# Kernel optimization log

Hardware: AMD Instinct MI355X
Metric: run time of the kernel (lower is better)

## Reference

```python
import jax, jax.numpy as jnp
import numpy as np

B, S, T = 2, 4096, 4096
SRC, DST, WIDTH = 512, 512, 128
BLK = 128  # JAKAL_ADDITIVE_ROUTE_BLOCK_SIZE default


def setup_inputs() -> dict:
    key = jax.random.key(0)
    ks = jax.random.split(key, 7)
    return {
        "source_val": jax.random.normal(ks[0], (B, S, SRC), jnp.float32),
        "target_val": jax.random.normal(ks[1], (B, T, DST), jnp.float32),
        "Ws": jax.random.normal(ks[2], (WIDTH, SRC), jnp.float32) * 0.02,  # source_proj weight
        "Wt": jax.random.normal(ks[3], (WIDTH, DST), jnp.float32) * 0.02,  # target_proj weight
        "ws_out": jax.random.normal(ks[4], (WIDTH,), jnp.float32) * 0.02,  # source_out weight
        "wt_out": jax.random.normal(ks[5], (WIDTH,), jnp.float32) * 0.02,  # target_out weight
        "w_int": jax.random.normal(ks[6], (WIDTH,), jnp.float32) * 0.02,   # interaction_weight
        "bias": jnp.zeros((), jnp.float32),
    }


def reference(source_val, target_val, Ws, Wt, ws_out, wt_out, w_int, bias):
    # Projections (Linear without bias): y = x @ W.T
    ps = jnp.einsum('bsd,wd->bsw', source_val, Ws)   # [B,S,WIDTH]
    pt = jnp.einsum('btd,wd->btw', target_val, Wt)   # [B,T,WIDTH]
    s_lin = jnp.einsum('bsw,w->bs', ps, ws_out)      # [B,S]
    t_lin = jnp.einsum('btw,w->bt', pt, wt_out)      # [B,T]

    nblk = S // BLK
    # Block the source axis, matching the torch block loop (avoids a [B,S,T,W] tensor).
    ps_blocks = ps.reshape(B, nblk, BLK, WIDTH).transpose(1, 0, 2, 3)   # [nblk,B,BLK,W]
    sl_blocks = s_lin.reshape(B, nblk, BLK).transpose(1, 0, 2)          # [nblk,B,BLK]

    def block_scores(_, xs):
        ps_blk, sl_blk = xs
        # SiLU of the elementwise bilinear interaction, then low-rank weighted reduce.
        inter = jax.nn.silu(ps_blk[:, :, None, :] * pt[:, None, :, :])  # [B,BLK,T,W]
        sc = jnp.einsum('bktw,w->bkt', inter, w_int)
        sc = sc + sl_blk[:, :, None] + t_lin[:, None, :] + bias
        return None, sc

    _, out = jax.lax.scan(block_scores, None, (ps_blocks, sl_blocks))   # [nblk,B,BLK,T]
    return out.transpose(1, 0, 2, 3).reshape(B, S, T)
```

## Files before the change

### kernel.cpp

```cpp
#include <hip/hip_runtime.h>
#include <cstdint>
#include <cstddef>

#define B_ 2
#define S_ 4096
#define T_ 4096
#define D_ 512
#define W_ 128

#define A0C (-0.0006958f)
#define A1C (0.2529946f)
#define A2C (-0.0226345f)
#define A3C (0.0022173f)
#define A4C (-0.00011668f)
#define ZCUT 2.5f
#define ROWCAP 65536

typedef __attribute__((ext_vector_type(8))) short bf16x8;
typedef __attribute__((ext_vector_type(4))) float f32x4;

__device__ __forceinline__ uint16_t f2bf(float f){
  uint32_t u = __float_as_uint(f);
  u += 0x7FFFu + ((u >> 16) & 1u);
  return (uint16_t)(u >> 16);
}
__device__ __forceinline__ float bf2f(uint16_t h){
  return __uint_as_float(((uint32_t)h) << 16);
}

__device__ __forceinline__ void gl_lds16(const void* g, void* l){
  __builtin_amdgcn_global_load_lds(
      (const __attribute__((address_space(1))) void*)g,
      (__attribute__((address_space(3))) void*)l, 16, 0, 0);
}

union F4 { float4 v; float f[4]; };

template<int INBF>
__global__ void prep_k(const void* __restrict__ Ws, const void* __restrict__ Wt,
                       const void* __restrict__ wso, const void* __restrict__ wto,
                       const void* __restrict__ wi, const void* __restrict__ bias,
                       float* __restrict__ WsT, float* __restrict__ WtT,
                       float* __restrict__ wsof, float* __restrict__ wtof,
                       float* __restrict__ wif, float* __restrict__ cbias,
                       float* __restrict__ maxT, int* __restrict__ rowCnt){
  auto cv = [](const void* p, int i)->float{
    if (INBF) return bf2f(((const uint16_t*)p)[i]);
    return ((const float*)p)[i];
  };
  const void* in = (blockIdx.x & 1) ? Wt : Ws;
  float* out = (blockIdx.x & 1) ? WtT : WsT;
  int base = (blockIdx.x >> 1) * 4096;
  for (int o = base + threadIdx.x; o < base + 4096; o += blockDim.x){
    int d = o >> 7, w = o & (W_ - 1);
    out[o] = cv(in, w * D_ + d);
  }
  if (blockIdx.x == 1){
    maxT[threadIdx.x] = 0.f;
  }
  if (blockIdx.x == 0){
    if (threadIdx.x < W_){
      wsof[threadIdx.x] = cv(wso, threadIdx.x);
      wtof[threadIdx.x] = cv(wto, threadIdx.x);
      wif[threadIdx.x]  = cv(wi,  threadIdx.x);
    }
    __syncthreads();
    if (threadIdx.x == 0){
      float s = 0.f;
      for (int k = 0; k < W_; ++k) s += wif[k];
      cbias[0] = cv(bias, 0) + A0C * s;
      rowCnt[0] = 0;
    }
  }
}

template<int INBF, int MODE>
__global__ __launch_bounds__(256) void proj_k(const void* __restrict__ xraw,
        const float* __restrict__ WT, const float* __restrict__ wout,
        const float* __restrict__ wint,
        float* __restrict__ pT, float* __restrict__ lin,
        uint16_t* __restrict__ feat, float* __restrict__ maxT){
  __shared__ float xl[64 * 18];
  __shared__ float wl[64 * 128];
  int tid = threadIdx.x;
  int tx = tid & 31, ty = tid >> 5;
  int rowBase = blockIdx.x * 16;
  float acc[2][4] = {};
  for (int c = 0; c < 8; ++c){
    int d0 = c * 64;
    const float4* wt4 = (const float4*)(WT + (size_t)d0 * W_);
    float4* wl4 = (float4*)wl;
    #pragma unroll
    for (int p = 0; p < 8; ++p){ int q = tid + 256 * p; wl4[q] = wt4[q]; }
    {
      int q = tid;
      int r = q >> 4, dq = q & 15;
      float v0, v1, v2, v3;
      if (INBF){
        const uint16_t* xp = (const uint16_t*)xraw + (size_t)(rowBase + r) * D_ + d0 + dq * 4;
        ushort4 u = *(const ushort4*)xp;
        v0 = bf2f(u.x); v1 = bf2f(u.y); v2 = bf2f(u.z); v3 = bf2f(u.w);
      } else {
        const float* xp = (const float*)xraw + (size_t)(rowBase + r) * D_ + d0 + dq * 4;
        float4 u = *(const float4*)xp;
        v0 = u.x; v1 = u.y; v2 = u.z; v3 = u.w;
      }
      xl[(dq*4+0)*18 + r] = v0;
      xl[(dq*4+1)*18 + r] = v1;
      xl[(dq*4+2)*18 + r] = v2;
      xl[(dq*4+3)*18 + r] = v3;
    }
    __syncthreads();
    #pragma unroll 4
    for (int d = 0; d < 64; ++d){
      float a0 = xl[d * 18 + ty * 2 + 0];
      float a1 = xl[d * 18 + ty * 2 + 1];
      F4 w;
      w.v = *(const float4*)(wl + d * 128 + tx * 4);
      #pragma unroll
      for (int j = 0; j < 4; ++j){
        acc[0][j] = fmaf(a0, w.f[j], acc[0][j]);
        acc[1][j] = fmaf(a1, w.f[j], acc[1][j]);
      }
    }
    __syncthreads();
  }
  float* tile = wl;
  #pragma unroll
  for (int i = 0; i < 2; ++i)
    #pragma unroll
    for (int j = 0; j < 4; ++j)
      tile[(tx*4 + j) * 17 + ty*2 + i] = acc[i][j];
  F4 wo; wo.v = *(const float4*)(wout + tx * 4);
  F4 wiv;
  if (MODE == 0) wiv.v = *(const float4*)(wint + tx * 4);
  #pragma unroll
  for (int i = 0; i < 2; ++i){
    int r = rowBase + ty * 2 + i;
    float s = acc[i][0]*wo.f[0] + acc[i][1]*wo.f[1] + acc[i][2]*wo.f[2] + acc[i][3]*wo.f[3];
    #pragma unroll
    for (int off = 16; off >= 1; off >>= 1) s += __shfl_xor(s, off, 32);
    if (tx == 0) lin[r] = s;
    ushort4 g[5];
    uint16_t* gp = (uint16_t*)g;
    #pragma unroll
    for (int j = 0; j < 4; ++j){
      float p = acc[i][j];
      float p2 = p*p, p4 = p2*p2, p6 = p4*p2, p8 = p4*p4;
      float e0, e1, e2, e3, e4;
      if (MODE == 0){
        float wq = wiv.f[j];
        e0 = 0.5f * wq * p; e1 = A1C * wq * p2; e2 = A2C * wq * p4;
        e3 = A3C * wq * p6; e4 = A4C * wq * p8;
      } else {
        e0 = p; e1 = p2; e2 = p4; e3 = p6; e4 = p8;
      }
      gp[0*4+j] = f2bf(e0); gp[1*4+j] = f2bf(e1); gp[2*4+j] = f2bf(e2);
      gp[3*4+j] = f2bf(e3); gp[4*4+j] = f2bf(e4);
    }
    uint16_t* o = feat + (size_t)r * 640 + tx * 4;
    *(ushort4*)(o)       = g[0];
    *(ushort4*)(o + 128) = g[1];
    *(ushort4*)(o + 256) = g[2];
    *(ushort4*)(o + 384) = g[3];
    *(ushort4*)(o + 512) = g[4];
  }
  __syncthreads();
  int b = rowBase >> 12;
  {
    int w = tid >> 1, h = tid & 1;
    int sb = rowBase & (S_ - 1);
    float* dst = pT + ((size_t)(b * W_ + w)) * S_ + sb + h * 8;
    const float* src = tile + w * 17 + h * 8;
    #pragma unroll
    for (int k = 0; k < 2; ++k){
      float4 o = make_float4(src[k*4+0], src[k*4+1], src[k*4+2], src[k*4+3]);
      *(float4*)(dst + k * 4) = o;
    }
  }
  if (MODE == 1 && tid < W_){
    int w = tid;
    float m = 0.f;
    #pragma unroll
    for (int r = 0; r < 16; ++r) m = fmaxf(m, fabsf(tile[w * 17 + r]));
    atomicMax((unsigned int*)&maxT[b * W_ + w], __float_as_uint(m));
  }
}

template<int OUTBF>
__global__ __launch_bounds__(512) void gemm_k(const uint16_t* __restrict__ fA,
      const uint16_t* __restrict__ fB, const float* __restrict__ slin,
      const float* __restrict__ tlin, const float* __restrict__ cbias,
      void* __restrict__ outv){
  __shared__ __align__(16) uint16_t As[2][256 * 32];
  __shared__ __align__(16) uint16_t Bs[2][256 * 32];
  int tid = threadIdx.x, lane = tid & 63, wv = tid >> 6;
  int quad = lane >> 4, lr = lane & 15;
  int wm = wv >> 2, wn = wv & 3;
  int sl = quad ^ ((lane >> 1) & 3);
  int rowT = blockIdx.y * 256, colT = blockIdx.x * 256;
  int bb = rowT >> 12;

  const uint16_t* aBase = fA + (size_t)rowT * 640;
  const uint16_t* bBase = fB + ((size_t)bb * T_ + colT) * 640;

  int srw = tid >> 2;
  int k0 = (((tid & 3) ^ ((tid >> 3) & 3))) * 8;

  f32x4 acc[8][4];
  #pragma unroll
  for (int i = 0; i < 8; ++i)
    #pragma unroll
    for (int j = 0; j < 4; ++j)
      acc[i][j] = (f32x4){0.f, 0.f, 0.f, 0.f};

  auto STAGE = [&](int tile){
    int sb = tile & 1;
    int kc = tile * 32;
    gl_lds16(aBase + (size_t)srw * 640 + kc + k0,         &As[sb][tid * 8]);
    gl_lds16(aBase + (size_t)(128 + srw) * 640 + kc + k0, &As[sb][4096 + tid * 8]);
    gl_lds16(bBase + (size_t)srw * 640 + kc + k0,         &Bs[sb][tid * 8]);
    gl_lds16(bBase + (size_t)(128 + srw) * 640 + kc + k0, &Bs[sb][4096 + tid * 8]);
  };

  STAGE(0);
  for (int tile = 0; tile < 20; ++tile){
    int buf = tile & 1;
    if (tile + 1 < 20){
      STAGE(tile + 1);
      asm volatile("s_waitcnt vmcnt(4)" ::: "memory");
    } else {
      asm volatile("s_waitcnt vmcnt(0)" ::: "memory");
    }
    __builtin_amdgcn_s_barrier();
    bf16x8 bq[4];
    #pragma unroll
    for (int nj = 0; nj < 4; ++nj)
      bq[nj] = *(const bf16x8*)&Bs[buf][(wn*64 + nj*16 + lr) * 32 + sl * 8];
    #pragma unroll
    for (int mi = 0; mi < 8; ++mi){
      bf16x8 aq = *(const bf16x8*)&As[buf][(wm*128 + mi*16 + lr) * 32 + sl * 8];
      #pragma unroll
      for (int nj = 0; nj < 4; ++nj)
        acc[mi][nj] = __builtin_amdgcn_mfma_f32_16x16x32_bf16(bq[nj], aq, acc[mi][nj], 0, 0, 0);
    }
    __builtin_amdgcn_s_barrier();
  }

  float cb = cbias[0];
  #pragma unroll
  for (int mi = 0; mi < 8; ++mi){
    int srow = rowT + wm * 128 + mi * 16 + lr;
    float sv = slin[srow] + cb;
    #pragma unroll
    for (int nj = 0; nj < 4; ++nj){
      int t0 = colT + wn * 64 + nj * 16 + quad * 4;
      F4 tl; tl.v = *(const float4*)(tlin + bb * T_ + t0);
      float o0 = acc[mi][nj][0] + sv + tl.f[0];
      float o1 = acc[mi][nj][1] + sv + tl.f[1];
      float o2 = acc[mi][nj][2] + sv + tl.f[2];
      float o3 = acc[mi][nj][3] + sv + tl.f[3];
      size_t oi = (size_t)srow * T_ + t0;
      if (OUTBF){
        ushort4 pk = make_ushort4(f2bf(o0), f2bf(o1), f2bf(o2), f2bf(o3));
        *(ushort4*)((uint16_t*)outv + oi) = pk;
      } else {
        *(float4*)((float*)outv + oi) = make_float4(o0, o1, o2, o3);
      }
    }
  }
}

__global__ void flagrows_k(const float* __restrict__ psT, const float* __restrict__ maxT,
                           uint32_t* __restrict__ rowList, int* __restrict__ rowCnt){
  int w = blockIdx.x, b = blockIdx.y;
  int tid = threadIdx.x;
  float mt = maxT[b * W_ + w];
  const float* psc = psT + (size_t)(b * W_ + w) * S_;
  for (int s = tid; s < S_; s += 256){
    float p = psc[s];
    if (fabsf(p) * mt > ZCUT){
      int k = atomicAdd(rowCnt, 1);
      if (k < ROWCAP)
        rowList[k] = ((uint32_t)b << 19) | ((uint32_t)w << 12) | (uint32_t)s;
    }
  }
}

template<int OUTBF>
__global__ __launch_bounds__(256) void fixscan_k(const float* __restrict__ psT,
        const float* __restrict__ ptT, const float* __restrict__ wint,
        const uint16_t* __restrict__ fA, const uint16_t* __restrict__ fB,
        const uint32_t* __restrict__ rowList, const int* __restrict__ rowCnt,
        void* __restrict__ outv){
  int n = *rowCnt; if (n > ROWCAP) n = ROWCAP;
  int tid = threadIdx.x;
  for (int job = blockIdx.x; job < n; job += gridDim.x){
    uint32_t pk = rowList[job];
    int b = (int)(pk >> 19), w = (int)((pk >> 12) & 127u), s = (int)(pk & 4095u);
    float wi = wint[w];
    float p = psT[(size_t)(b * W_ + w) * S_ + s];
    const float* ptc = ptT + (size_t)(b * W_ + w) * T_;
    const uint16_t* fa = fA + ((size_t)b * S_ + s) * 640 + w;
    float a0 = bf2f(fa[0]),   a1 = bf2f(fa[128]), a2 = bf2f(fa[256]);
    float a3 = bf2f(fa[384]), a4 = bf2f(fa[512]);
    for (int t = tid; t < T_; t += 256){
      float q = ptc[t];
      float z = p * q;
      if (fabsf(z) > ZCUT){
        const uint16_t* fb = fB + ((size_t)b * T_ + t) * 640 + w;
        float dot = a0 * bf2f(fb[0]) + a1 * bf2f(fb[128]) + a2 * bf2f(fb[256])
                  + a3 * bf2f(fb[384]) + a4 * bf2f(fb[512]);
        float sil = z / (1.0f + __expf(-z));
        float corr = wi * sil - dot - A0C * wi;
        size_t idx = ((size_t)b * S_ + s) * T_ + t;
        if (OUTBF){
          uint32_t* wp = (uint32_t*)outv + (idx >> 1);
          bool hi = (idx & 1u) != 0;
          uint32_t assumed, old = *wp;
          do {
            assumed = old;
            uint16_t h = hi ? (uint16_t)(assumed >> 16) : (uint16_t)(assumed & 0xFFFFu);
            uint16_t nh = f2bf(bf2f(h) + corr);
            uint32_t nw = hi ? ((assumed & 0x0000FFFFu) | ((uint32_t)nh << 16))
                             : ((assumed & 0xFFFF0000u) | (uint32_t)nh);
            old = atomicCAS(wp, assumed, nw);
          } while (old != assumed);
        } else {
          atomicAdd((float*)outv + idx, corr);
        }
      }
    }
  }
}

extern "C" void kernel_launch(void* const* d_in, const int* in_sizes, int n_in,
                              void* d_out, int out_size, void* d_ws, size_t ws_size,
                              hipStream_t stream){
  char* ws = (char*)d_ws;
  size_t off = 0;
  auto alloc = [&](size_t bytes)->char*{
    char* p = ws + off; off += (bytes + 255) & ~(size_t)255; return p;
  };
  float*    WsT  = (float*)   alloc((size_t)D_*W_*4);
  float*    WtT  = (float*)   alloc((size_t)D_*W_*4);
  float*    wsof = (float*)   alloc(W_*4);
  float*    wtof = (float*)   alloc(W_*4);
  float*    wif  = (float*)   alloc(W_*4);
  float*    cbias= (float*)   alloc(4);
  int*      rowCnt=(int*)     alloc(4);
  uint32_t* rowList=(uint32_t*)alloc((size_t)ROWCAP*4);
  float*    psT  = (float*)   alloc((size_t)B_*S_*W_*4);
  float*    ptT  = (float*)   alloc((size_t)B_*T_*W_*4);
  float*    slin = (float*)   alloc((size_t)B_*S_*4);
  float*    tlin = (float*)   alloc((size_t)B_*T_*4);
  float*    maxT = (float*)   alloc((size_t)B_*W_*4);
  uint16_t* featA= (uint16_t*)alloc((size_t)B_*S_*640*2);
  uint16_t* featB= (uint16_t*)alloc((size_t)B_*T_*640*2);

  bool inbf  = (in_sizes[0] == (int)((size_t)B_*S_*D_*2));
  bool outbf = (out_size    == (int)((size_t)B_*S_*T_*2));

  if (inbf){
    hipLaunchKernelGGL((prep_k<1>), dim3(32), dim3(256), 0, stream,
        d_in[2], d_in[3], d_in[4], d_in[5], d_in[6], d_in[7],
        WsT, WtT, wsof, wtof, wif, cbias, maxT, rowCnt);
    hipLaunchKernelGGL((proj_k<1,0>), dim3(B_*S_/16), dim3(256), 0, stream,
        d_in[0], WsT, wsof, wif, psT, slin, featA, maxT);
    hipLaunchKernelGGL((proj_k<1,1>), dim3(B_*T_/16), dim3(256), 0, stream,
        d_in[1], WtT, wtof, wif, ptT, tlin, featB, maxT);
  } else {
    hipLaunchKernelGGL((prep_k<0>), dim3(32), dim3(256), 0, stream,
        d_in[2], d_in[3], d_in[4], d_in[5], d_in[6], d_in[7],
        WsT, WtT, wsof, wtof, wif, cbias, maxT, rowCnt);
    hipLaunchKernelGGL((proj_k<0,0>), dim3(B_*S_/16), dim3(256), 0, stream,
        d_in[0], WsT, wsof, wif, psT, slin, featA, maxT);
    hipLaunchKernelGGL((proj_k<0,1>), dim3(B_*T_/16), dim3(256), 0, stream,
        d_in[1], WtT, wtof, wif, ptT, tlin, featB, maxT);
  }
  if (outbf)
    hipLaunchKernelGGL((gemm_k<1>), dim3(T_/256, B_*S_/256), dim3(512), 0, stream,
        featA, featB, slin, tlin, cbias, d_out);
  else
    hipLaunchKernelGGL((gemm_k<0>), dim3(T_/256, B_*S_/256), dim3(512), 0, stream,
        featA, featB, slin, tlin, cbias, d_out);
  hipLaunchKernelGGL(flagrows_k, dim3(W_, B_), dim3(256), 0, stream,
      psT, maxT, rowList, rowCnt);
  if (outbf)
    hipLaunchKernelGGL((fixscan_k<1>), dim3(2048), dim3(256), 0, stream,
        psT, ptT, wif, featA, featB, rowList, rowCnt, d_out);
  else
    hipLaunchKernelGGL((fixscan_k<0>), dim3(2048), dim3(256), 0, stream,
        psT, ptT, wif, featA, featB, rowList, rowCnt, d_out);
}
```

Baseline: 308.4 us.

## Merge source/target projection launches and XCD-swizzle GEMM tile order

The two projection launches are merged into one 1024-block launch, with the source or target mode chosen at runtime from the block index. This removes a kernel launch and lets both halves run concurrently. The GEMM now remaps its linear block id so each XCD gets an 8x8 group of neighbouring output tiles, meant to improve L2 reuse of the A and B feature panels. The risk is that the runtime mode branch adds some divergence and register pressure to the projection kernel.

```diff
diff --git a/kernel.cpp b/kernel.cpp
--- a/kernel.cpp
+++ b/kernel.cpp
@@ -74,17 +74,28 @@
   }
 }
 
-template<int INBF, int MODE>
-__global__ __launch_bounds__(256) void proj_k(const void* __restrict__ xraw,
-        const float* __restrict__ WT, const float* __restrict__ wout,
+template<int INBF>
+__global__ __launch_bounds__(256) void proj_k(
+        const void* __restrict__ xrawS, const void* __restrict__ xrawT,
+        const float* __restrict__ WsT, const float* __restrict__ WtT,
+        const float* __restrict__ wsof, const float* __restrict__ wtof,
         const float* __restrict__ wint,
-        float* __restrict__ pT, float* __restrict__ lin,
-        uint16_t* __restrict__ feat, float* __restrict__ maxT){
+        float* __restrict__ psT, float* __restrict__ ptT,
+        float* __restrict__ slin, float* __restrict__ tlin,
+        uint16_t* __restrict__ featA, uint16_t* __restrict__ featB,
+        float* __restrict__ maxT){
   __shared__ float xl[64 * 18];
   __shared__ float wl[64 * 128];
   int tid = threadIdx.x;
   int tx = tid & 31, ty = tid >> 5;
-  int rowBase = blockIdx.x * 16;
+  int mode = (blockIdx.x >= 512) ? 1 : 0;
+  const void* xraw = mode ? xrawT : xrawS;
+  const float* WT  = mode ? WtT : WsT;
+  const float* wout= mode ? wtof : wsof;
+  float* pT        = mode ? ptT : psT;
+  float* lin       = mode ? tlin : slin;
+  uint16_t* feat   = mode ? featB : featA;
+  int rowBase = (blockIdx.x & 511) * 16;
   float acc[2][4] = {};
   for (int c = 0; c < 8; ++c){
     int d0 = c * 64;
@@ -133,7 +144,7 @@
       tile[(tx*4 + j) * 17 + ty*2 + i] = acc[i][j];
   F4 wo; wo.v = *(const float4*)(wout + tx * 4);
   F4 wiv;
-  if (MODE == 0) wiv.v = *(const float4*)(wint + tx * 4);
+  if (mode == 0) wiv.v = *(const float4*)(wint + tx * 4);
   #pragma unroll
   for (int i = 0; i < 2; ++i){
     int r = rowBase + ty * 2 + i;
@@ -148,7 +159,7 @@
       float p = acc[i][j];
       float p2 = p*p, p4 = p2*p2, p6 = p4*p2, p8 = p4*p4;
       float e0, e1, e2, e3, e4;
-      if (MODE == 0){
+      if (mode == 0){
         float wq = wiv.f[j];
         e0 = 0.5f * wq * p; e1 = A1C * wq * p2; e2 = A2C * wq * p4;
         e3 = A3C * wq * p6; e4 = A4C * wq * p8;
@@ -178,7 +189,7 @@
       *(float4*)(dst + k * 4) = o;
     }
   }
-  if (MODE == 1 && tid < W_){
+  if (mode == 1 && tid < W_){
     int w = tid;
     float m = 0.f;
     #pragma unroll
@@ -198,7 +209,12 @@
   int quad = lane >> 4, lr = lane & 15;
   int wm = wv >> 2, wn = wv & 3;
   int sl = quad ^ ((lane >> 1) & 3);
-  int rowT = blockIdx.y * 256, colT = blockIdx.x * 256;
+
+  int bid = blockIdx.y * gridDim.x + blockIdx.x;
+  int xcd = bid & 7, idx = bid >> 3;
+  int bx = (xcd & 1) * 8 + (idx & 7);
+  int by = (xcd >> 1) * 8 + (idx >> 3);
+  int rowT = by * 256, colT = bx * 256;
   int bb = rowT >> 12;
 
   const uint16_t* aBase = fA + (size_t)rowT * 640;
@@ -365,18 +381,16 @@
     hipLaunchKernelGGL((prep_k<1>), dim3(32), dim3(256), 0, stream,
         d_in[2], d_in[3], d_in[4], d_in[5], d_in[6], d_in[7],
         WsT, WtT, wsof, wtof, wif, cbias, maxT, rowCnt);
-    hipLaunchKernelGGL((proj_k<1,0>), dim3(B_*S_/16), dim3(256), 0, stream,
-        d_in[0], WsT, wsof, wif, psT, slin, featA, maxT);
-    hipLaunchKernelGGL((proj_k<1,1>), dim3(B_*T_/16), dim3(256), 0, stream,
-        d_in[1], WtT, wtof, wif, ptT, tlin, featB, maxT);
+    hipLaunchKernelGGL((proj_k<1>), dim3(1024), dim3(256), 0, stream,
+        d_in[0], d_in[1], WsT, WtT, wsof, wtof, wif,
+        psT, ptT, slin, tlin, featA, featB, maxT);
   } else {
     hipLaunchKernelGGL((prep_k<0>), dim3(32), dim3(256), 0, stream,
         d_in[2], d_in[3], d_in[4], d_in[5], d_in[6], d_in[7],
         WsT, WtT, wsof, wtof, wif, cbias, maxT, rowCnt);
-    hipLaunchKernelGGL((proj_k<0,0>), dim3(B_*S_/16), dim3(256), 0, stream,
-        d_in[0], WsT, wsof, wif, psT, slin, featA, maxT);
-    hipLaunchKernelGGL((proj_k<0,1>), dim3(B_*T_/16), dim3(256), 0, stream,
-        d_in[1], WtT, wtof, wif, ptT, tlin, featB, maxT);
+    hipLaunchKernelGGL((proj_k<0>), dim3(1024), dim3(256), 0, stream,
+        d_in[0], d_in[1], WsT, WtT, wsof, wtof, wif,
+        psT, ptT, slin, tlin, featA, featB, maxT);
   }
   if (outbf)
     hipLaunchKernelGGL((gemm_k<1>), dim3(T_/256, B_*S_/256), dim3(512), 0, stream,
```

Result: faster. 300.9 us (-2.4%).
